# Kernel tuning notes

Measured on AMD Instinct MI355X. Metric: run time of the kernel, lower is better.

The kernel has to match this reference:

```python
import jax, jax.numpy as jnp
import numpy as np

H = 16          # num_heads
DK = 64         # k_dim_head
DV = 64         # v_dim_head
DIM = 1024      # model dim (= H*DK = H*DV)


def _split_heads(x, h):
    # ... T (H d) -> ... H T d
    x = x.reshape(x.shape[:-1] + (h, -1))
    return jnp.swapaxes(x, -2, -3)


def _merge_heads(x):
    # ... H T d -> ... T (H d)
    x = jnp.swapaxes(x, -2, -3)
    return x.reshape(x.shape[:-2] + (-1,))


def setup_inputs() -> dict:
    key = jax.random.key(0)
    ks = jax.random.split(key, 8)
    B, T = 2, 2048
    q = jax.random.normal(ks[0], (B, T, DIM), dtype=jnp.float32)
    k = jax.random.normal(ks[1], (B, T, DIM), dtype=jnp.float32)
    v = jax.random.normal(ks[2], (B, T, DIM), dtype=jnp.float32)
    # causal boolean mask [T, T] (True = attend)
    mask = jnp.tril(jnp.ones((T, T), dtype=bool))
    s = 1.0 / np.sqrt(DIM)
    # weights stored as [in, out] so projection is x @ W (== torch Linear, no bias)
    Wq = jax.random.normal(ks[3], (DIM, H * DK), dtype=jnp.float32) * s
    Wk = jax.random.normal(ks[4], (DIM, H * DK), dtype=jnp.float32) * s
    Wv = jax.random.normal(ks[5], (DIM, H * DV), dtype=jnp.float32) * s
    Wo = jax.random.normal(ks[6], (H * DV, DIM), dtype=jnp.float32) * s
    return {"q": q, "k": k, "v": v, "mask": mask,
            "Wq": Wq, "Wk": Wk, "Wv": Wv, "Wo": Wo}


def reference(q, k, v, mask, Wq, Wk, Wv, Wo):
    q_i = _split_heads(q @ Wq, H)                       # ... H T dk
    k_i = _split_heads(k @ Wk, H)                       # ... H T dk
    v_i = _split_heads(v @ Wv, H)                       # ... H T dv
    s_qk = jnp.einsum('...hik,...hjk->...hij', q_i, k_i) / jnp.sqrt(
        jnp.asarray(DK, dtype=q_i.dtype))               # ... H T T
    neg = -jnp.finfo(s_qk.dtype).max
    s_qk = jnp.where(mask, s_qk, neg)
    attn = jax.nn.softmax(s_qk, axis=-1)
    vals = jnp.einsum('...hij,...hjv->...hiv', attn, v_i)
    return _merge_heads(vals) @ Wo                      # ... T out_dim
```

## Files before the change

kernel.cpp:

```cpp
#include <hip/hip_runtime.h>
#include <hip/hip_bf16.h>
#include <stdint.h>

#define T_SEQ  2048
#define DMODEL 1024
#define NBATCH 2
#define NHEAD  16
#define DHEAD  64
#define MTOT   (NBATCH * T_SEQ)

typedef __attribute__((ext_vector_type(8))) short short8_t;
typedef __attribute__((ext_vector_type(4))) float f32x4;
typedef __attribute__((ext_vector_type(2))) __bf16 bhalf2_t;
typedef __attribute__((ext_vector_type(4))) uint32_t uint4_t;

typedef const __attribute__((address_space(1))) void* gas_t;
typedef __attribute__((address_space(3))) void* las_t;

__device__ __forceinline__ ushort f2bf(float f) {
    return __builtin_bit_cast(unsigned short, (__bf16)f);
}
__device__ __forceinline__ uint32_t pk_bf16(float a, float b) {
    bhalf2_t t; t[0] = (__bf16)a; t[1] = (__bf16)b;
    return __builtin_bit_cast(uint32_t, t);
}

__global__ __launch_bounds__(256) void convert_qkv_kernel(
        const float* __restrict__ q, const float* __restrict__ k,
        const float* __restrict__ v, ushort* __restrict__ outb) {
    const size_t per = (size_t)MTOT * DMODEL / 4;
    size_t idx = (size_t)blockIdx.x * 256 + threadIdx.x;
    int t = (int)(idx / per);
    size_t i = idx - (size_t)t * per;
    const float4* src = (const float4*)(t == 0 ? q : (t == 1 ? k : v));
    float4 val = src[i];
    uint2 o;
    o.x = pk_bf16(val.x, val.y);
    o.y = pk_bf16(val.z, val.w);
    ((uint2*)outb)[(size_t)t * per + i] = o;
}

__global__ __launch_bounds__(256) void convw_kernel(
        const float* __restrict__ Wq, const float* __restrict__ Wk,
        const float* __restrict__ Wv, const float* __restrict__ Wo,
        ushort* __restrict__ wt) {
    __shared__ float tile[32][33];
    int z = blockIdx.z;
    const float* W = z == 0 ? Wq : z == 1 ? Wk : z == 2 ? Wv : Wo;
    const float sc = (z == 0) ? 0.18033688011f : 1.0f;
    ushort* out = wt + (size_t)z * DMODEL * DMODEL;
    int tx = threadIdx.x, ty = threadIdx.y;
    int k0 = blockIdx.x * 32, n0 = blockIdx.y * 32;
    #pragma unroll
    for (int i = 0; i < 4; i++)
        tile[ty + i * 8][tx] = W[(size_t)(k0 + ty + i * 8) * DMODEL + n0 + tx];
    __syncthreads();
    #pragma unroll
    for (int i = 0; i < 4; i++)
        out[(size_t)(n0 + ty + i * 8) * DMODEL + k0 + tx] = f2bf(tile[tx][ty + i * 8] * sc);
}

template <bool OUT_F32>
__global__ __launch_bounds__(256, 2) void gemm_bt_kernel(
        const ushort* __restrict__ Aall, const ushort* __restrict__ Btall,
        void* __restrict__ Call, int M, int N, int K) {
    const ushort* A  = Aall  + (size_t)blockIdx.z * M * K;
    const ushort* Bt = Btall + (size_t)blockIdx.z * N * K;

    __shared__ ushort As[128 * 32];
    __shared__ ushort Bs[128 * 32];

    const int tid  = threadIdx.x;
    const int lane = tid & 63;
    const int wid  = tid >> 6;
    const int wr = wid >> 1, wc = wid & 1;
    const int m_base = blockIdx.x * 128;
    const int n_base = blockIdx.y * 128;

    f32x4 acc[4][4] = {};

    const int srow = lane >> 2;
    const int scol = (lane & 3) * 8;

    for (int kk = 0; kk < K; kk += 32) {
        __syncthreads();
        #pragma unroll
        for (int i = 0; i < 2; i++) {
            int c = wid * 2 + i;
            const ushort* ga = A  + (size_t)(m_base + c * 16 + srow) * K + kk + scol;
            const ushort* gb = Bt + (size_t)(n_base + c * 16 + srow) * K + kk + scol;
            __builtin_amdgcn_global_load_lds((gas_t)ga, (las_t)(As + c * 512), 16, 0, 0);
            __builtin_amdgcn_global_load_lds((gas_t)gb, (las_t)(Bs + c * 512), 16, 0, 0);
        }
        __syncthreads();
        short8_t a[4], b[4];
        #pragma unroll
        for (int mt = 0; mt < 4; mt++)
            a[mt] = *(const short8_t*)(As + (wr * 64 + mt * 16 + (lane & 15)) * 32 + (lane >> 4) * 8);
        #pragma unroll
        for (int nt = 0; nt < 4; nt++)
            b[nt] = *(const short8_t*)(Bs + (wc * 64 + nt * 16 + (lane & 15)) * 32 + (lane >> 4) * 8);
        #pragma unroll
        for (int mt = 0; mt < 4; mt++)
            #pragma unroll
            for (int nt = 0; nt < 4; nt++)
                acc[mt][nt] = __builtin_amdgcn_mfma_f32_16x16x32_bf16(a[mt], b[nt], acc[mt][nt], 0, 0, 0);
    }

    const int row0 = m_base + wr * 64 + (lane >> 4) * 4;
    const int col0 = n_base + wc * 64 + (lane & 15);
    if constexpr (OUT_F32) {
        float* C = (float*)Call + (size_t)blockIdx.z * M * N;
        #pragma unroll
        for (int mt = 0; mt < 4; mt++)
            #pragma unroll
            for (int nt = 0; nt < 4; nt++)
                #pragma unroll
                for (int r = 0; r < 4; r++)
                    C[(size_t)(row0 + mt * 16 + r) * N + col0 + nt * 16] = acc[mt][nt][r];
    } else {
        ushort* C = (ushort*)Call + (size_t)blockIdx.z * M * N;
        #pragma unroll
        for (int mt = 0; mt < 4; mt++)
            #pragma unroll
            for (int nt = 0; nt < 4; nt++)
                #pragma unroll
                for (int r = 0; r < 4; r++)
                    C[(size_t)(row0 + mt * 16 + r) * N + col0 + nt * 16] = f2bf(acc[mt][nt][r]);
    }
}

__global__ __launch_bounds__(256, 2) void attn_kernel(
        const ushort* __restrict__ Qp, const ushort* __restrict__ Kp,
        const ushort* __restrict__ Vp, ushort* __restrict__ Op) {
    __shared__ __attribute__((aligned(16))) ushort Ksh[2][64 * 72];
    __shared__ __attribute__((aligned(16))) ushort Vts[2][64 * 72];
    __shared__ __attribute__((aligned(16))) ushort Psh[4][16 * 72];

    const int tid = threadIdx.x, lane = tid & 63, w = tid >> 6;
    const int g = lane >> 4;
    const int m = lane & 15;
    const int bh = blockIdx.y;
    const int b = bh >> 4, h = bh & 15;

    const ushort* Qb = Qp + (size_t)(b * T_SEQ) * DMODEL + h * DHEAD;
    const ushort* Kb = Kp + (size_t)(b * T_SEQ) * DMODEL + h * DHEAD;
    const ushort* Vb = Vp + (size_t)(b * T_SEQ) * DMODEL + h * DHEAD;
    ushort* Ob = Op + (size_t)(b * T_SEQ) * DMODEL + h * DHEAD;

    const int qa = blockIdx.x;
    const int na = qa + 1;

    const int kr  = tid >> 3, kck = (tid & 7) * 8;
    const int kvp = tid & 31, dvc = tid >> 5;

    short8_t kreg0, kreg1, vreg0, vreg1;
    auto LOADKV = [&](int kv0) {
        kreg0 = *(const short8_t*)(Kb + (size_t)(kv0 + kr) * DMODEL + kck);
        kreg1 = *(const short8_t*)(Kb + (size_t)(kv0 + kr + 32) * DMODEL + kck);
        const ushort* vsrc = Vb + (size_t)(kv0 + kvp * 2) * DMODEL + dvc * 8;
        vreg0 = *(const short8_t*)(vsrc);
        vreg1 = *(const short8_t*)(vsrc + DMODEL);
    };
    auto WRITEKV = [&](int buf) {
        *(short8_t*)(&Ksh[buf][kr * 72 + kck]) = kreg0;
        *(short8_t*)(&Ksh[buf][(kr + 32) * 72 + kck]) = kreg1;
        uint4_t a = __builtin_bit_cast(uint4_t, vreg0);
        uint4_t c = __builtin_bit_cast(uint4_t, vreg1);
        #pragma unroll
        for (int j = 0; j < 4; j++) {
            uint32_t pk0 = __builtin_amdgcn_perm(c[j], a[j], 0x05040100u);
            uint32_t pk1 = __builtin_amdgcn_perm(c[j], a[j], 0x07060302u);
            *(uint32_t*)(&Vts[buf][(dvc * 8 + 2 * j) * 72 + kvp * 2]) = pk0;
            *(uint32_t*)(&Vts[buf][(dvc * 8 + 2 * j + 1) * 72 + kvp * 2]) = pk1;
        }
    };

    int qi = qa, q0 = qa * 64;
    short8_t qf[2];
    #pragma unroll
    for (int kc = 0; kc < 2; kc++)
        qf[kc] = *(const short8_t*)(Qb + (size_t)(q0 + w * 16 + m) * DMODEL + kc * 32 + g * 8);

    f32x4 acc_o[4] = {};
    float mrun = -1e30f, lrun = 0.f;
    ushort* Pw = Psh[w];

    auto WRITE_O = [&]() {
        #pragma unroll
        for (int r = 0; r < 4; r++) {
            float linv = __builtin_amdgcn_rcpf(__shfl(lrun, g * 4 + r));
            int qrow = q0 + w * 16 + g * 4 + r;
            #pragma unroll
            for (int dt = 0; dt < 4; dt++)
                Ob[(size_t)qrow * DMODEL + dt * 16 + m] = f2bf(acc_o[dt][r] * linv);
        }
    };
    auto TILE = [&](int t) { return (t < na) ? t : t - na; };

    LOADKV(TILE(0) * 64);
    WRITEKV(0);
    LOADKV(TILE(1) * 64);

    for (int tt = 0; tt < 33; ++tt) {
        if (tt == na) {
            WRITE_O();
            #pragma unroll
            for (int dt = 0; dt < 4; dt++) acc_o[dt] = f32x4{0.f, 0.f, 0.f, 0.f};
            mrun = -1e30f; lrun = 0.f;
            qi = 31 - qa; q0 = qi * 64;
            #pragma unroll
            for (int kc = 0; kc < 2; kc++)
                qf[kc] = *(const short8_t*)(Qb + (size_t)(q0 + w * 16 + m) * DMODEL + kc * 32 + g * 8);
        }
        const int t = TILE(tt);
        const int kv0 = t * 64;
        const bool need_mask = (t == qi);
        const int cur = tt & 1;

        __syncthreads();
        if (tt + 1 < 33) {
            WRITEKV(cur ^ 1);
            if (tt + 2 < 33) LOADKV(TILE(tt + 2) * 64);
        }

        f32x4 s[4] = {};
        __builtin_amdgcn_s_setprio(1);
        #pragma unroll
        for (int kvT = 0; kvT < 4; kvT++)
            #pragma unroll
            for (int kc = 0; kc < 2; kc++) {
                short8_t kf = *(const short8_t*)(&Ksh[cur][(kvT * 16 + m) * 72 + kc * 32 + g * 8]);
                s[kvT] = __builtin_amdgcn_mfma_f32_16x16x32_bf16(kf, qf[kc], s[kvT], 0, 0, 0);
            }
        __builtin_amdgcn_s_setprio(0);

        const int qg = q0 + w * 16 + m;
        float pmax = -1e30f;
        #pragma unroll
        for (int kvT = 0; kvT < 4; kvT++)
            #pragma unroll
            for (int r = 0; r < 4; r++) {
                float val = s[kvT][r];
                if (need_mask) {
                    int kv_g = kv0 + kvT * 16 + g * 4 + r;
                    if (kv_g > qg) val = -1e30f;
                }
                s[kvT][r] = val;
                pmax = fmaxf(pmax, val);
            }
        pmax = fmaxf(pmax, __shfl_xor(pmax, 16));
        pmax = fmaxf(pmax, __shfl_xor(pmax, 32));
        if (!__all(pmax <= mrun + 8.f)) {
            float mnew = fmaxf(mrun, pmax);
            float fac = exp2f(mrun - mnew);
            mrun = mnew;
            lrun *= fac;
            #pragma unroll
            for (int r = 0; r < 4; r++) {
                float f = __shfl(fac, g * 4 + r);
                #pragma unroll
                for (int dt = 0; dt < 4; dt++) acc_o[dt][r] *= f;
            }
        }
        float psum = 0.f;
        #pragma unroll
        for (int kvT = 0; kvT < 4; kvT++)
            #pragma unroll
            for (int r = 0; r < 4; r++) {
                float p = exp2f(s[kvT][r] - mrun);
                s[kvT][r] = p;
                psum += p;
            }
        psum += __shfl_xor(psum, 16);
        psum += __shfl_xor(psum, 32);
        lrun += psum;

        #pragma unroll
        for (int kvT = 0; kvT < 4; kvT++) {
            uint2 pk;
            pk.x = pk_bf16(s[kvT][0], s[kvT][1]);
            pk.y = pk_bf16(s[kvT][2], s[kvT][3]);
            *(uint2*)(Pw + m * 72 + kvT * 16 + g * 4) = pk;
        }

        short8_t pf[2];
        #pragma unroll
        for (int kc = 0; kc < 2; kc++)
            pf[kc] = *(const short8_t*)(Pw + m * 72 + kc * 32 + g * 8);
        __builtin_amdgcn_s_setprio(1);
        #pragma unroll
        for (int dt = 0; dt < 4; dt++)
            #pragma unroll
            for (int kc = 0; kc < 2; kc++) {
                short8_t vf = *(const short8_t*)(&Vts[cur][(dt * 16 + m) * 72 + kc * 32 + g * 8]);
                acc_o[dt] = __builtin_amdgcn_mfma_f32_16x16x32_bf16(pf[kc], vf, acc_o[dt], 0, 0, 0);
            }
        __builtin_amdgcn_s_setprio(0);
    }
    WRITE_O();
}

extern "C" void kernel_launch(void* const* d_in, const int* in_sizes, int n_in,
                              void* d_out, int out_size, void* d_ws, size_t ws_size,
                              hipStream_t stream) {
    (void)in_sizes; (void)n_in; (void)out_size; (void)ws_size;
    const float* q  = (const float*)d_in[0];
    const float* k  = (const float*)d_in[1];
    const float* v  = (const float*)d_in[2];
    const float* Wq = (const float*)d_in[4];
    const float* Wk = (const float*)d_in[5];
    const float* Wv = (const float*)d_in[6];
    const float* Wo = (const float*)d_in[7];

    ushort* ws = (ushort*)d_ws;
    const size_t MK = (size_t)MTOT * DMODEL;
    const size_t NK = (size_t)DMODEL * DMODEL;
    ushort* qkvb = ws;
    ushort* wt   = ws + 3 * MK;
    ushort* qkvp = ws + 3 * MK + 4 * NK;
    ushort* Op   = ws;

    convert_qkv_kernel<<<dim3(12288), dim3(256), 0, stream>>>(q, k, v, qkvb);
    convw_kernel<<<dim3(32, 32, 4), dim3(32, 8), 0, stream>>>(Wq, Wk, Wv, Wo, wt);
    gemm_bt_kernel<false><<<dim3(32, 8, 3), dim3(256), 0, stream>>>(qkvb, wt, (void*)qkvp,
                                                                    MTOT, DMODEL, DMODEL);
    attn_kernel<<<dim3(16, 32), dim3(256), 0, stream>>>(qkvp, qkvp + MK, qkvp + 2 * MK, Op);
    gemm_bt_kernel<true><<<dim3(32, 8, 1), dim3(256), 0, stream>>>(Op, wt + 3 * NK, d_out,
                                                                   MTOT, DMODEL, DMODEL);
}
```

Measured before the change: 133.9 us.

## Rewrite attention with 32x32 MFMA, register-resident P, and per-tile blocks

The attention kernel now uses 32x32x16 bf16 MFMAs with 2 waves per block, each covering 32 query rows. The softmax probabilities stay in registers as the A operand of the PV MFMA, which removes the LDS round trip for P. The V tile is written to LDS with a permuted key order so the accumulator layout lines up with the operand layout. Blocks no longer pair a short and a long query tile for load balance; each block handles one query tile, launched longest first, giving twice as many smaller blocks.

After: 149.2 us. 1.11x slower.

```diff
diff --git a/kernel.cpp b/kernel.cpp
--- a/kernel.cpp
+++ b/kernel.cpp
@@ -11,6 +11,7 @@
 
 typedef __attribute__((ext_vector_type(8))) short short8_t;
 typedef __attribute__((ext_vector_type(4))) float f32x4;
+typedef __attribute__((ext_vector_type(16))) float f32x16;
 typedef __attribute__((ext_vector_type(2))) __bf16 bhalf2_t;
 typedef __attribute__((ext_vector_type(4))) uint32_t uint4_t;
 
@@ -23,6 +24,16 @@
 __device__ __forceinline__ uint32_t pk_bf16(float a, float b) {
     bhalf2_t t; t[0] = (__bf16)a; t[1] = (__bf16)b;
     return __builtin_bit_cast(uint32_t, t);
+}
+
+template <int B>
+__device__ __forceinline__ short8_t pack8(const f32x16 &s) {
+    uint4_t u;
+    u[0] = pk_bf16(s[B + 0], s[B + 1]);
+    u[1] = pk_bf16(s[B + 2], s[B + 3]);
+    u[2] = pk_bf16(s[B + 4], s[B + 5]);
+    u[3] = pk_bf16(s[B + 6], s[B + 7]);
+    return __builtin_bit_cast(short8_t, u);
 }
 
 __global__ __launch_bounds__(256) void convert_qkv_kernel(
@@ -130,16 +141,14 @@
     }
 }
 
-__global__ __launch_bounds__(256, 2) void attn_kernel(
+__global__ __launch_bounds__(128, 2) void attn_kernel(
         const ushort* __restrict__ Qp, const ushort* __restrict__ Kp,
         const ushort* __restrict__ Vp, ushort* __restrict__ Op) {
     __shared__ __attribute__((aligned(16))) ushort Ksh[2][64 * 72];
     __shared__ __attribute__((aligned(16))) ushort Vts[2][64 * 72];
-    __shared__ __attribute__((aligned(16))) ushort Psh[4][16 * 72];
 
     const int tid = threadIdx.x, lane = tid & 63, w = tid >> 6;
-    const int g = lane >> 4;
-    const int m = lane & 15;
+    const int m31 = lane & 31, hi = lane >> 5;
     const int bh = blockIdx.y;
     const int b = bh >> 4, h = bh & 15;
 
@@ -148,157 +157,151 @@
     const ushort* Vb = Vp + (size_t)(b * T_SEQ) * DMODEL + h * DHEAD;
     ushort* Ob = Op + (size_t)(b * T_SEQ) * DMODEL + h * DHEAD;
 
-    const int qa = blockIdx.x;
-    const int na = qa + 1;
-
-    const int kr  = tid >> 3, kck = (tid & 7) * 8;
-    const int kvp = tid & 31, dvc = tid >> 5;
-
-    short8_t kreg0, kreg1, vreg0, vreg1;
+    const int qi = 31 - (int)blockIdx.x;
+    const int nt = qi + 1;
+    const int q0 = qi * 64;
+    const int q0w = q0 + w * 32;
+    const int qg = q0w + m31;
+
+    const int kr = tid >> 1, kc64 = (tid & 1) * 32;
+    const int kvp = tid & 31, dvs = tid >> 5;
+    const int lp = kvp & 7, q2 = lp >> 1;
+    const int q2p = ((q2 & 1) << 1) | (q2 >> 1);
+    const int kvc = (kvp & ~7) | (q2p << 1) | (lp & 1);
+
+    short8_t kreg[4], vreg[4];
     auto LOADKV = [&](int kv0) {
-        kreg0 = *(const short8_t*)(Kb + (size_t)(kv0 + kr) * DMODEL + kck);
-        kreg1 = *(const short8_t*)(Kb + (size_t)(kv0 + kr + 32) * DMODEL + kck);
-        const ushort* vsrc = Vb + (size_t)(kv0 + kvp * 2) * DMODEL + dvc * 8;
-        vreg0 = *(const short8_t*)(vsrc);
-        vreg1 = *(const short8_t*)(vsrc + DMODEL);
+        #pragma unroll
+        for (int j = 0; j < 4; j++)
+            kreg[j] = *(const short8_t*)(Kb + (size_t)(kv0 + kr) * DMODEL + kc64 + j * 8);
+        const ushort* vsrc = Vb + (size_t)(kv0 + kvp * 2) * DMODEL + dvs * 16;
+        vreg[0] = *(const short8_t*)(vsrc);
+        vreg[1] = *(const short8_t*)(vsrc + 8);
+        vreg[2] = *(const short8_t*)(vsrc + DMODEL);
+        vreg[3] = *(const short8_t*)(vsrc + DMODEL + 8);
     };
     auto WRITEKV = [&](int buf) {
-        *(short8_t*)(&Ksh[buf][kr * 72 + kck]) = kreg0;
-        *(short8_t*)(&Ksh[buf][(kr + 32) * 72 + kck]) = kreg1;
-        uint4_t a = __builtin_bit_cast(uint4_t, vreg0);
-        uint4_t c = __builtin_bit_cast(uint4_t, vreg1);
-        #pragma unroll
-        for (int j = 0; j < 4; j++) {
-            uint32_t pk0 = __builtin_amdgcn_perm(c[j], a[j], 0x05040100u);
-            uint32_t pk1 = __builtin_amdgcn_perm(c[j], a[j], 0x07060302u);
-            *(uint32_t*)(&Vts[buf][(dvc * 8 + 2 * j) * 72 + kvp * 2]) = pk0;
-            *(uint32_t*)(&Vts[buf][(dvc * 8 + 2 * j + 1) * 72 + kvp * 2]) = pk1;
+        #pragma unroll
+        for (int j = 0; j < 4; j++)
+            *(short8_t*)(&Ksh[buf][kr * 72 + kc64 + j * 8]) = kreg[j];
+        #pragma unroll
+        for (int c = 0; c < 2; c++) {
+            uint4_t a = __builtin_bit_cast(uint4_t, vreg[c]);
+            uint4_t o = __builtin_bit_cast(uint4_t, vreg[2 + c]);
+            #pragma unroll
+            for (int j = 0; j < 4; j++) {
+                int d0 = dvs * 16 + c * 8 + 2 * j;
+                *(uint32_t*)(&Vts[buf][(d0 + 0) * 72 + kvc * 2]) =
+                    __builtin_amdgcn_perm(o[j], a[j], 0x05040100u);
+                *(uint32_t*)(&Vts[buf][(d0 + 1) * 72 + kvc * 2]) =
+                    __builtin_amdgcn_perm(o[j], a[j], 0x07060302u);
+            }
         }
     };
 
-    int qi = qa, q0 = qa * 64;
-    short8_t qf[2];
+    short8_t qf[4];
     #pragma unroll
-    for (int kc = 0; kc < 2; kc++)
-        qf[kc] = *(const short8_t*)(Qb + (size_t)(q0 + w * 16 + m) * DMODEL + kc * 32 + g * 8);
-
-    f32x4 acc_o[4] = {};
+    for (int dkc = 0; dkc < 4; dkc++)
+        qf[dkc] = *(const short8_t*)(Qb + (size_t)(q0w + m31) * DMODEL + dkc * 16 + hi * 8);
+
+    f32x16 acc0 = {}, acc1 = {};
     float mrun = -1e30f, lrun = 0.f;
-    ushort* Pw = Psh[w];
-
-    auto WRITE_O = [&]() {
-        #pragma unroll
-        for (int r = 0; r < 4; r++) {
-            float linv = __builtin_amdgcn_rcpf(__shfl(lrun, g * 4 + r));
-            int qrow = q0 + w * 16 + g * 4 + r;
-            #pragma unroll
-            for (int dt = 0; dt < 4; dt++)
-                Ob[(size_t)qrow * DMODEL + dt * 16 + m] = f2bf(acc_o[dt][r] * linv);
-        }
-    };
-    auto TILE = [&](int t) { return (t < na) ? t : t - na; };
-
-    LOADKV(TILE(0) * 64);
+
+    LOADKV(0);
     WRITEKV(0);
-    LOADKV(TILE(1) * 64);
-
-    for (int tt = 0; tt < 33; ++tt) {
-        if (tt == na) {
-            WRITE_O();
-            #pragma unroll
-            for (int dt = 0; dt < 4; dt++) acc_o[dt] = f32x4{0.f, 0.f, 0.f, 0.f};
-            mrun = -1e30f; lrun = 0.f;
-            qi = 31 - qa; q0 = qi * 64;
-            #pragma unroll
-            for (int kc = 0; kc < 2; kc++)
-                qf[kc] = *(const short8_t*)(Qb + (size_t)(q0 + w * 16 + m) * DMODEL + kc * 32 + g * 8);
-        }
-        const int t = TILE(tt);
+    LOADKV(64);
+
+    for (int t = 0; t < nt; ++t) {
         const int kv0 = t * 64;
-        const bool need_mask = (t == qi);
-        const int cur = tt & 1;
+        const int cur = t & 1;
+        const bool need_mask = (t == nt - 1);
 
         __syncthreads();
-        if (tt + 1 < 33) {
+        if (t + 1 < nt) {
             WRITEKV(cur ^ 1);
-            if (tt + 2 < 33) LOADKV(TILE(tt + 2) * 64);
-        }
-
-        f32x4 s[4] = {};
+            if (t + 2 < nt) LOADKV((t + 2) * 64);
+        }
+
+        f32x16 s0 = {}, s1 = {};
         __builtin_amdgcn_s_setprio(1);
         #pragma unroll
-        for (int kvT = 0; kvT < 4; kvT++)
-            #pragma unroll
-            for (int kc = 0; kc < 2; kc++) {
-                short8_t kf = *(const short8_t*)(&Ksh[cur][(kvT * 16 + m) * 72 + kc * 32 + g * 8]);
-                s[kvT] = __builtin_amdgcn_mfma_f32_16x16x32_bf16(kf, qf[kc], s[kvT], 0, 0, 0);
+        for (int dkc = 0; dkc < 4; dkc++) {
+            short8_t kf0 = *(const short8_t*)(&Ksh[cur][(m31) * 72 + dkc * 16 + hi * 8]);
+            short8_t kf1 = *(const short8_t*)(&Ksh[cur][(32 + m31) * 72 + dkc * 16 + hi * 8]);
+            s0 = __builtin_amdgcn_mfma_f32_32x32x16_bf16(kf0, qf[dkc], s0, 0, 0, 0);
+            s1 = __builtin_amdgcn_mfma_f32_32x32x16_bf16(kf1, qf[dkc], s1, 0, 0, 0);
+        }
+        __builtin_amdgcn_s_setprio(0);
+
+        if (need_mask) {
+            const int kvb = kv0 + 4 * hi;
+            #pragma unroll
+            for (int r = 0; r < 16; r++) {
+                int kvl = (r & 3) + 8 * (r >> 2);
+                if (kvb + kvl      > qg) s0[r] = -1e30f;
+                if (kvb + kvl + 32 > qg) s1[r] = -1e30f;
             }
-        __builtin_amdgcn_s_setprio(0);
-
-        const int qg = q0 + w * 16 + m;
-        float pmax = -1e30f;
-        #pragma unroll
-        for (int kvT = 0; kvT < 4; kvT++)
-            #pragma unroll
-            for (int r = 0; r < 4; r++) {
-                float val = s[kvT][r];
-                if (need_mask) {
-                    int kv_g = kv0 + kvT * 16 + g * 4 + r;
-                    if (kv_g > qg) val = -1e30f;
-                }
-                s[kvT][r] = val;
-                pmax = fmaxf(pmax, val);
-            }
-        pmax = fmaxf(pmax, __shfl_xor(pmax, 16));
-        pmax = fmaxf(pmax, __shfl_xor(pmax, 32));
+        }
+
+        float tm[16];
+        #pragma unroll
+        for (int r = 0; r < 16; r++) tm[r] = fmaxf(s0[r], s1[r]);
+        #pragma unroll
+        for (int st = 8; st >= 1; st >>= 1)
+            #pragma unroll
+            for (int i = 0; i < st; i++) tm[i] = fmaxf(tm[i], tm[i + st]);
+        float pmax = fmaxf(tm[0], __shfl_xor(tm[0], 32));
+
         if (!__all(pmax <= mrun + 8.f)) {
             float mnew = fmaxf(mrun, pmax);
             float fac = exp2f(mrun - mnew);
             mrun = mnew;
             lrun *= fac;
             #pragma unroll
-            for (int r = 0; r < 4; r++) {
-                float f = __shfl(fac, g * 4 + r);
-                #pragma unroll
-                for (int dt = 0; dt < 4; dt++) acc_o[dt][r] *= f;
+            for (int r = 0; r < 16; r++) {
+                float fr = __shfl(fac, (r & 3) + 8 * (r >> 2) + 4 * hi);
+                acc0[r] *= fr; acc1[r] *= fr;
             }
         }
-        float psum = 0.f;
-        #pragma unroll
-        for (int kvT = 0; kvT < 4; kvT++)
-            #pragma unroll
-            for (int r = 0; r < 4; r++) {
-                float p = exp2f(s[kvT][r] - mrun);
-                s[kvT][r] = p;
-                psum += p;
-            }
-        psum += __shfl_xor(psum, 16);
-        psum += __shfl_xor(psum, 32);
-        lrun += psum;
-
-        #pragma unroll
-        for (int kvT = 0; kvT < 4; kvT++) {
-            uint2 pk;
-            pk.x = pk_bf16(s[kvT][0], s[kvT][1]);
-            pk.y = pk_bf16(s[kvT][2], s[kvT][3]);
-            *(uint2*)(Pw + m * 72 + kvT * 16 + g * 4) = pk;
-        }
-
-        short8_t pf[2];
-        #pragma unroll
-        for (int kc = 0; kc < 2; kc++)
-            pf[kc] = *(const short8_t*)(Pw + m * 72 + kc * 32 + g * 8);
+
+        float ps[16];
+        #pragma unroll
+        for (int r = 0; r < 16; r++) {
+            s0[r] = exp2f(s0[r] - mrun);
+            s1[r] = exp2f(s1[r] - mrun);
+            ps[r] = s0[r] + s1[r];
+        }
+        #pragma unroll
+        for (int st = 8; st >= 1; st >>= 1)
+            #pragma unroll
+            for (int i = 0; i < st; i++) ps[i] += ps[i + st];
+        lrun += ps[0] + __shfl_xor(ps[0], 32);
+
+        short8_t pa[4];
+        pa[0] = pack8<0>(s0);
+        pa[1] = pack8<8>(s0);
+        pa[2] = pack8<0>(s1);
+        pa[3] = pack8<8>(s1);
         __builtin_amdgcn_s_setprio(1);
         #pragma unroll
-        for (int dt = 0; dt < 4; dt++)
-            #pragma unroll
-            for (int kc = 0; kc < 2; kc++) {
-                short8_t vf = *(const short8_t*)(&Vts[cur][(dt * 16 + m) * 72 + kc * 32 + g * 8]);
-                acc_o[dt] = __builtin_amdgcn_mfma_f32_16x16x32_bf16(pf[kc], vf, acc_o[dt], 0, 0, 0);
-            }
+        for (int ks = 0; ks < 4; ks++) {
+            short8_t vf0 = *(const short8_t*)(&Vts[cur][(m31) * 72 + ks * 16 + hi * 8]);
+            short8_t vf1 = *(const short8_t*)(&Vts[cur][(32 + m31) * 72 + ks * 16 + hi * 8]);
+            acc0 = __builtin_amdgcn_mfma_f32_32x32x16_bf16(pa[ks], vf0, acc0, 0, 0, 0);
+            acc1 = __builtin_amdgcn_mfma_f32_32x32x16_bf16(pa[ks], vf1, acc1, 0, 0, 0);
+        }
         __builtin_amdgcn_s_setprio(0);
     }
-    WRITE_O();
+
+    float linv = __builtin_amdgcn_rcpf(lrun);
+    #pragma unroll
+    for (int r = 0; r < 16; r++) {
+        int ql = (r & 3) + 8 * (r >> 2) + 4 * hi;
+        float li = __shfl(linv, ql);
+        ushort* orow = Ob + (size_t)(q0w + ql) * DMODEL + m31;
+        orow[0]  = f2bf(acc0[r] * li);
+        orow[32] = f2bf(acc1[r] * li);
+    }
 }
 
 extern "C" void kernel_launch(void* const* d_in, const int* in_sizes, int n_in,
@@ -325,7 +328,7 @@
     convw_kernel<<<dim3(32, 32, 4), dim3(32, 8), 0, stream>>>(Wq, Wk, Wv, Wo, wt);
     gemm_bt_kernel<false><<<dim3(32, 8, 3), dim3(256), 0, stream>>>(qkvb, wt, (void*)qkvp,
                                                                     MTOT, DMODEL, DMODEL);
-    attn_kernel<<<dim3(16, 32), dim3(256), 0, stream>>>(qkvp, qkvp + MK, qkvp + 2 * MK, Op);
+    attn_kernel<<<dim3(32, 32), dim3(128), 0, stream>>>(qkvp, qkvp + MK, qkvp + 2 * MK, Op);
     gemm_bt_kernel<true><<<dim3(32, 8, 1), dim3(256), 0, stream>>>(Op, wt + 3 * NK, d_out,
                                                                    MTOT, DMODEL, DMODEL);
 }
```
